# Performance work log

Hardware: AMD Instinct MI355X
Metric: run time of the kernel (lower is better)

Reference implementation:

```python
import jax, jax.numpy as jnp
import numpy as np

B, S, D, H = 4, 2048, 768, 12
HD = D // H
SCALE = HD ** -0.5


def setup_inputs() -> dict:
    key = jax.random.key(0)
    ks = jax.random.split(key, 9)
    std = D ** -0.5
    x = jax.random.normal(ks[0], (B, S, D), dtype=jnp.float32)
    Wq = jax.random.normal(ks[1], (D, D), dtype=jnp.float32) * std
    Wk = jax.random.normal(ks[2], (D, D), dtype=jnp.float32) * std
    Wv = jax.random.normal(ks[3], (D, D), dtype=jnp.float32) * std
    Wo = jax.random.normal(ks[4], (D, D), dtype=jnp.float32) * std
    bq = jax.random.normal(ks[5], (D,), dtype=jnp.float32) * 0.01
    bk = jax.random.normal(ks[6], (D,), dtype=jnp.float32) * 0.01
    bv = jax.random.normal(ks[7], (D,), dtype=jnp.float32) * 0.01
    bo = jax.random.normal(ks[8], (D,), dtype=jnp.float32) * 0.01
    return {"x": x, "Wq": Wq, "bq": bq, "Wk": Wk, "bk": bk,
            "Wv": Wv, "bv": bv, "Wo": Wo, "bo": bo}


def reference(x, Wq, bq, Wk, bk, Wv, bv, Wo, bo):
    b, s, _ = x.shape
    # projections (torch Linear: y = x @ W.T + b)
    q = (x @ Wq.T + bq).reshape(b, s, H, HD).transpose(0, 2, 1, 3)  # [B,H,S,HD]
    k = (x @ Wk.T + bk).reshape(b, s, H, HD).transpose(0, 2, 1, 3)
    v = (x @ Wv.T + bv).reshape(b, s, H, HD).transpose(0, 2, 1, 3)
    attn = jnp.einsum('bhqd,bhkd->bhqk', q, k) * SCALE
    attn = jax.nn.softmax(attn, axis=-1)  # dropout is identity in eval mode
    out = jnp.einsum('bhqk,bhkd->bhqd', attn, v)
    out = out.transpose(0, 2, 1, 3).reshape(b, s, D)
    return out @ Wo.T + bo
```

## Files before the change

### kernel.cpp

```cpp
#include <hip/hip_runtime.h>

#define LOG2E 1.4426950408889634f
#define QSCALE (0.125f * LOG2E)

typedef __attribute__((ext_vector_type(8))) __bf16 bf8_t;
typedef __attribute__((ext_vector_type(4))) float f4_t;

__device__ __forceinline__ unsigned short f2bf(float f) {
  unsigned int u = __float_as_uint(f);
  u += 0x7fff + ((u >> 16) & 1);
  return (unsigned short)(u >> 16);
}

__device__ __forceinline__ void async16(const void* g, void* l) {
  __builtin_amdgcn_global_load_lds(
      (const __attribute__((address_space(1))) void*)g,
      (__attribute__((address_space(3))) void*)l, 16, 0, 0);
}

__device__ __forceinline__ int swm(int r) {
  return ((r & 3) << 4) | ((r & 8) << 3);
}
__device__ __forceinline__ int swzoff(int row, int cb) {
  return (row << 7) + (cb ^ swm(row));
}

__global__ void cvt_multi(const float* __restrict__ x,
                          const float* __restrict__ w0, const float* __restrict__ w1,
                          const float* __restrict__ w2, const float* __restrict__ w3,
                          unsigned short* __restrict__ xb,
                          unsigned short* __restrict__ d0, unsigned short* __restrict__ d1,
                          unsigned short* __restrict__ d2, unsigned short* __restrict__ d3) {
  const int NX = 1572864;
  const int NW = 147456;
  const int total = NX + 4 * NW;
  int i = blockIdx.x * blockDim.x + threadIdx.x;
  int stride = gridDim.x * blockDim.x;
  for (; i < total; i += stride) {
    const float* s;
    unsigned short* d;
    int off;
    if (i < NX) {
      s = x; d = xb; off = i;
    } else {
      int j = i - NX;
      int wsel = j / NW;
      off = j - wsel * NW;
      s = (wsel == 0) ? w0 : (wsel == 1) ? w1 : (wsel == 2) ? w2 : w3;
      d = (wsel == 0) ? d0 : (wsel == 1) ? d1 : (wsel == 2) ? d2 : d3;
    }
    float4 v = ((const float4*)s)[off];
    ushort4 o;
    o.x = f2bf(v.x); o.y = f2bf(v.y); o.z = f2bf(v.z); o.w = f2bf(v.w);
    ((ushort4*)d)[off] = o;
  }
}

__device__ __forceinline__ void gemm_core(const unsigned short* __restrict__ A,
                                          const unsigned short* __restrict__ Bm,
                                          int i0, int j0, char* ls,
                                          f4_t (&acc)[4][4]) {
  const int tid = threadIdx.x;
  const int l = tid & 63;
  const int wi = (tid >> 6) >> 1, wj = (tid >> 6) & 1;
  auto stage = [&](int buf, int k0) {
    char* dA = ls + buf * 32768;
    char* dB = dA + 16384;
#pragma unroll
    for (int u = 0; u < 4; ++u) {
      int p = (u * 256 + tid) * 16;
      int r = p >> 7, c = (p & 127) ^ swm(r);
      async16((const char*)A + ((size_t)(i0 + r) * 768 + k0) * 2 + c, dA + p);
      async16((const char*)Bm + ((size_t)(j0 + r) * 768 + k0) * 2 + c, dB + p);
    }
  };
  stage(0, 0);
  __syncthreads();
  for (int kk = 0; kk < 12; ++kk) {
    if (kk < 11) stage((kk + 1) & 1, (kk + 1) * 64);
    const char* lsA = ls + (kk & 1) * 32768;
    const char* lsB = lsA + 16384;
#pragma unroll
    for (int ks = 0; ks < 2; ++ks) {
      bf8_t af[4], bfr[4];
#pragma unroll
      for (int mi = 0; mi < 4; ++mi)
        af[mi] = *(const bf8_t*)(lsA + swzoff(wi * 64 + mi * 16 + (l & 15),
                                              ks * 64 + ((l >> 4) << 4)));
#pragma unroll
      for (int nj = 0; nj < 4; ++nj)
        bfr[nj] = *(const bf8_t*)(lsB + swzoff(wj * 64 + nj * 16 + (l & 15),
                                               ks * 64 + ((l >> 4) << 4)));
      __builtin_amdgcn_s_setprio(1);
#pragma unroll
      for (int mi = 0; mi < 4; ++mi)
#pragma unroll
        for (int nj = 0; nj < 4; ++nj)
          acc[mi][nj] = __builtin_amdgcn_mfma_f32_16x16x32_bf16(
              af[mi], bfr[nj], acc[mi][nj], 0, 0, 0);
      __builtin_amdgcn_s_setprio(0);
    }
    __syncthreads();
  }
}

__global__ __launch_bounds__(256) void proj_qkv(
    const unsigned short* __restrict__ xb,
    const unsigned short* __restrict__ wq,
    const unsigned short* __restrict__ wk,
    const unsigned short* __restrict__ wv,
    const float* __restrict__ bq, const float* __restrict__ bk,
    const float* __restrict__ bv,
    unsigned short* __restrict__ qo, unsigned short* __restrict__ ko,
    unsigned short* __restrict__ vto) {
  __shared__ char ls[65536];
  const int bx = (blockIdx.x & 7) * 144 + (blockIdx.x >> 3);
  const int mt = bx / 18, nt = bx % 18;
  const int sec = nt / 6, nn = nt % 6;
  const int nbase = nn * 128;
  const int mbase = mt * 128;
  const unsigned short *A, *Bm;
  if (sec == 0)      { A = wq; Bm = xb; }
  else if (sec == 1) { A = wk; Bm = xb; }
  else               { A = xb; Bm = wv; }
  const int gi0 = (sec == 2) ? mbase : nbase;
  const int gj0 = (sec == 2) ? nbase : mbase;
  f4_t acc[4][4] = {};
  gemm_core(A, Bm, gi0, gj0, ls, acc);

  const int tid = threadIdx.x, l = tid & 63;
  const int wi = (tid >> 6) >> 1, wj = (tid >> 6) & 1;
#pragma unroll
  for (int mi = 0; mi < 4; ++mi) {
#pragma unroll
    for (int nj = 0; nj < 4; ++nj) {
      int ib = wi * 64 + mi * 16 + ((l >> 4) << 2);
      int j  = wj * 64 + nj * 16 + (l & 15);
      f4_t v = acc[mi][nj];
      ushort4 o;
      if (sec < 2) {
        const float* bias = sec ? bk : bq;
        float sc = sec ? 1.0f : QSCALE;
        float4 bs = *(const float4*)(bias + nbase + ib);
        o.x = f2bf((v[0] + bs.x) * sc);
        o.y = f2bf((v[1] + bs.y) * sc);
        o.z = f2bf((v[2] + bs.z) * sc);
        o.w = f2bf((v[3] + bs.w) * sc);
      } else {
        float bvs = bv[nbase + j];
        o.x = f2bf(v[0] + bvs); o.y = f2bf(v[1] + bvs);
        o.z = f2bf(v[2] + bvs); o.w = f2bf(v[3] + bvs);
      }
      int chunk = (ib >> 3) ^ (j & 15);
      *(ushort4*)(ls + j * 256 + chunk * 16 + ((ib & 7) << 1)) = o;
    }
  }
  __syncthreads();
  const int row = tid >> 1, half = tid & 1;
  if (sec < 2) {
    int sg = mbase + row;
    int b = sg >> 11, s = sg & 2047;
    int h = nn * 2 + half;
    unsigned short* dst = (sec ? ko : qo) + (((size_t)(b * 12 + h) * 2048 + s) << 6);
#pragma unroll
    for (int c = 0; c < 8; ++c) {
      int cb = half * 8 + c;
      uint4 v = *(const uint4*)(ls + row * 256 + ((cb ^ (row & 15)) << 4));
      ((uint4*)dst)[c] = v;
    }
  } else {
    int h = nn * 2 + (row >> 6), dh = row & 63;
    int b = mt >> 4;
    int scol = (mt & 15) * 128 + half * 64;
    unsigned short* dst = vto + ((size_t)((b * 12 + h) * 64 + dh)) * 2048 + scol;
#pragma unroll
    for (int c = 0; c < 8; ++c) {
      int cb = half * 8 + c;
      uint4 v = *(const uint4*)(ls + row * 256 + ((cb ^ (row & 15)) << 4));
      ((uint4*)dst)[c] = v;
    }
  }
}

__global__ __launch_bounds__(256) void proj_o(
    const unsigned short* __restrict__ attnb, const unsigned short* __restrict__ wo,
    const float* __restrict__ bo, float* __restrict__ outp) {
  __shared__ char ls[65536];
  const int bx = (blockIdx.x & 7) * 48 + (blockIdx.x >> 3);
  const int it = bx % 6, jt = bx / 6;
  const int i0 = it * 128, j0 = jt * 128;
  f4_t acc[4][4] = {};
  gemm_core(wo, attnb, i0, j0, ls, acc);
  const int tid = threadIdx.x, l = tid & 63;
  const int wi = (tid >> 6) >> 1, wj = (tid >> 6) & 1;
#pragma unroll
  for (int mi = 0; mi < 4; ++mi) {
#pragma unroll
    for (int nj = 0; nj < 4; ++nj) {
      int ib = i0 + wi * 64 + mi * 16 + ((l >> 4) << 2);
      int j  = j0 + wj * 64 + nj * 16 + (l & 15);
      float4 bs = *(const float4*)(bo + ib);
      float4 o;
      o.x = acc[mi][nj][0] + bs.x;
      o.y = acc[mi][nj][1] + bs.y;
      o.z = acc[mi][nj][2] + bs.z;
      o.w = acc[mi][nj][3] + bs.w;
      *(float4*)(outp + (size_t)j * 768 + ib) = o;
    }
  }
}

__global__ __launch_bounds__(512) void attn_kernel(
    const unsigned short* __restrict__ qg,
    const unsigned short* __restrict__ kg,
    const unsigned short* __restrict__ vtg,
    unsigned short* __restrict__ attnb) {
  __shared__ char ls[65536];
  const int tid = threadIdx.x, l = tid & 63, w = tid >> 6;
  const int qw = w & 3, hf = w >> 2;
  const int swz = (blockIdx.x & 7) * 96 + (blockIdx.x >> 3);
  const int q0 = (swz & 15) * 128;
  const int bh = swz >> 4;
  const size_t qkbase = (size_t)bh * 2048 * 64;
  const size_t vtbase = (size_t)bh * 64 * 2048;

#pragma unroll
  for (int u = 0; u < 2; ++u) {
    int p = (u * 512 + tid) * 16;
    int r = p >> 7, cb = p & 127;
    int c = cb ^ swm(r);
    async16((const char*)qg + (qkbase + (size_t)(q0 + r) * 64) * 2 + c, ls + p);
  }
  __syncthreads();
  bf8_t qf[2][2];
#pragma unroll
  for (int qt = 0; qt < 2; ++qt)
#pragma unroll
    for (int ks = 0; ks < 2; ++ks)
      qf[qt][ks] = *(const bf8_t*)(ls + swzoff(qw * 32 + qt * 16 + (l & 15),
                                               ks * 64 + ((l >> 4) << 4)));
  __syncthreads();

  const int p16 = tid * 16;
  const int sr = p16 >> 7;
  const int sc = (p16 & 127) ^ swm(sr);
  async16((const char*)kg + (qkbase + (size_t)sr * 64) * 2 + sc, ls + p16);
  async16((const char*)vtg + (vtbase + (size_t)sr * 2048) * 2 + sc,
          ls + 8192 + p16);
  async16((const char*)kg + (qkbase + (size_t)(64 + sr) * 64) * 2 + sc,
          ls + 16384 + p16);
  async16((const char*)vtg + (vtbase + (size_t)sr * 2048 + 64) * 2 + sc,
          ls + 16384 + 8192 + p16);
  const char* gKa = (const char*)kg + (qkbase + (size_t)(128 + sr) * 64) * 2 + sc;
  const char* gVa = (const char*)vtg + (vtbase + (size_t)sr * 2048 + 128) * 2 + sc;
  const char* gKb = gKa + 8192;
  const char* gVb = gVa + 128;
  __syncthreads();

  int koff[4][2];
#pragma unroll
  for (int kt = 0; kt < 4; ++kt) {
    int i = l & 15;
    int row = ((kt >> 1) << 5) + ((kt & 1) << 2) + ((i >> 2) << 3) + (i & 3);
#pragma unroll
    for (int ks = 0; ks < 2; ++ks)
      koff[kt][ks] = swzoff(row, ks * 64 + ((l >> 4) << 4));
  }
  int voff[4][2];
#pragma unroll
  for (int dt = 0; dt < 4; ++dt)
#pragma unroll
    for (int ks = 0; ks < 2; ++ks)
      voff[dt][ks] = swzoff(dt * 16 + (l & 15), ks * 64 + ((l >> 4) << 4));

  bf8_t onesf;
#pragma unroll
  for (int e = 0; e < 8; ++e) onesf[e] = (__bf16)1.0f;

  f4_t acc[4][2] = {};
  f4_t accs[2] = {};

  for (int i = 0; i < 16; ++i) {
    if (i < 15) {
      char* dst = ls + (((i + 1) & 1) * 2) * 16384;
      async16(gKa, dst + p16);
      async16(gVa, dst + 8192 + p16);
      async16(gKb, dst + 16384 + p16);
      async16(gVb, dst + 16384 + 8192 + p16);
      gKa += 16384; gKb += 16384;
      gVa += 256;   gVb += 256;
    }
    const char* bK = ls + ((i & 1) * 2 + hf) * 16384;
    const char* bV = bK + 8192;

    f4_t sacc[4][2] = {};
    __builtin_amdgcn_s_setprio(1);
#pragma unroll
    for (int kt = 0; kt < 4; ++kt)
#pragma unroll
      for (int ks = 0; ks < 2; ++ks) {
        bf8_t a = *(const bf8_t*)(bK + koff[kt][ks]);
#pragma unroll
        for (int qt = 0; qt < 2; ++qt)
          sacc[kt][qt] = __builtin_amdgcn_mfma_f32_16x16x32_bf16(
              a, qf[qt][ks], sacc[kt][qt], 0, 0, 0);
      }
    __builtin_amdgcn_s_setprio(0);

    bf8_t pf[2][2];
#pragma unroll
    for (int qt = 0; qt < 2; ++qt)
#pragma unroll
      for (int ks = 0; ks < 2; ++ks)
#pragma unroll
        for (int e = 0; e < 8; ++e)
          pf[ks][qt][e] =
              (__bf16)__builtin_amdgcn_exp2f(sacc[2 * ks + (e >> 2)][qt][e & 3]);

    __builtin_amdgcn_s_setprio(1);
#pragma unroll
    for (int dt = 0; dt < 4; ++dt) {
      bf8_t av0 = *(const bf8_t*)(bV + voff[dt][0]);
      bf8_t av1 = *(const bf8_t*)(bV + voff[dt][1]);
#pragma unroll
      for (int qt = 0; qt < 2; ++qt) {
        acc[dt][qt] = __builtin_amdgcn_mfma_f32_16x16x32_bf16(av0, pf[0][qt],
                                                              acc[dt][qt], 0, 0, 0);
        acc[dt][qt] = __builtin_amdgcn_mfma_f32_16x16x32_bf16(av1, pf[1][qt],
                                                              acc[dt][qt], 0, 0, 0);
      }
    }
#pragma unroll
    for (int qt = 0; qt < 2; ++qt) {
      accs[qt] = __builtin_amdgcn_mfma_f32_16x16x32_bf16(onesf, pf[0][qt],
                                                         accs[qt], 0, 0, 0);
      accs[qt] = __builtin_amdgcn_mfma_f32_16x16x32_bf16(onesf, pf[1][qt],
                                                         accs[qt], 0, 0, 0);
    }
    __builtin_amdgcn_s_setprio(0);
    __syncthreads();
  }

  char* reg_ = ls + qw * 8704;
  if (hf) {
#pragma unroll
    for (int dt = 0; dt < 4; ++dt)
#pragma unroll
      for (int qt = 0; qt < 2; ++qt)
        *(f4_t*)(reg_ + (((dt * 2 + qt) * 64) + l) * 16) = acc[dt][qt];
    *(float2*)(reg_ + 8192 + l * 8) = float2{accs[0][0], accs[1][0]};
  }
  __syncthreads();
  if (!hf) {
    const int bb = bh / 12, h = bh % 12;
    float2 os = *(const float2*)(reg_ + 8192 + l * 8);
    float inv0 = 1.0f / (accs[0][0] + os.x);
    float inv1 = 1.0f / (accs[1][0] + os.y);
#pragma unroll
    for (int qt = 0; qt < 2; ++qt) {
      float inv = qt ? inv1 : inv0;
      int s = q0 + qw * 32 + qt * 16 + (l & 15);
#pragma unroll
      for (int dt = 0; dt < 4; ++dt) {
        f4_t other = *(const f4_t*)(reg_ + (((dt * 2 + qt) * 64) + l) * 16);
        int dg = h * 64 + dt * 16 + ((l >> 4) << 2);
        ushort4 o;
        o.x = f2bf((acc[dt][qt][0] + other[0]) * inv);
        o.y = f2bf((acc[dt][qt][1] + other[1]) * inv);
        o.z = f2bf((acc[dt][qt][2] + other[2]) * inv);
        o.w = f2bf((acc[dt][qt][3] + other[3]) * inv);
        *(ushort4*)(attnb + ((size_t)(bb * 2048 + s)) * 768 + dg) = o;
      }
    }
  }
}

extern "C" void kernel_launch(void* const* d_in, const int* in_sizes, int n_in,
                              void* d_out, int out_size, void* d_ws, size_t ws_size,
                              hipStream_t stream) {
  const float* x  = (const float*)d_in[0];
  const float* Wq = (const float*)d_in[1];
  const float* bq = (const float*)d_in[2];
  const float* Wk = (const float*)d_in[3];
  const float* bk = (const float*)d_in[4];
  const float* Wv = (const float*)d_in[5];
  const float* bv = (const float*)d_in[6];
  const float* Wo = (const float*)d_in[7];
  const float* bo = (const float*)d_in[8];

  const size_t XB_ELEMS = (size_t)8192 * 768;
  const size_t W_ELEMS  = (size_t)768 * 768;
  unsigned short* xb  = (unsigned short*)d_ws;
  unsigned short* wqb = xb  + XB_ELEMS;
  unsigned short* wkb = wqb + W_ELEMS;
  unsigned short* wvb = wkb + W_ELEMS;
  unsigned short* wob = wvb + W_ELEMS;
  unsigned short* qb  = wob + W_ELEMS;
  unsigned short* kb  = qb  + XB_ELEMS;
  unsigned short* vtb = kb  + XB_ELEMS;
  unsigned short* attnb = xb;

  cvt_multi<<<2048, 256, 0, stream>>>(x, Wq, Wk, Wv, Wo,
                                      xb, wqb, wkb, wvb, wob);
  proj_qkv<<<1152, 256, 0, stream>>>(xb, wqb, wkb, wvb, bq, bk, bv, qb, kb, vtb);
  attn_kernel<<<768, 512, 0, stream>>>(qb, kb, vtb, attnb);
  proj_o<<<384, 256, 0, stream>>>(attnb, wob, bo, (float*)d_out);
}
```

Before: 138.1 us.

## Fuse fp32-to-bf16 conversion of x into QKV projection GEMM loads

The x activation is no longer converted to bf16 in a separate kernel. The QKV projection now loads fp32 x tiles into registers, converts them to bf16 and writes them into swizzled LDS, overlapping this with the MFMA work, while weights still use async LDS loads. This removes the full bf16 write and re-read of x, but each x tile is now read in fp32 by all 18 column tiles, which raises global read traffic. The shared gemm_core also replaces __syncthreads with explicit vmcnt waits plus s_barrier.

```diff
diff --git a/kernel.cpp b/kernel.cpp
--- a/kernel.cpp
+++ b/kernel.cpp
@@ -25,34 +25,102 @@
   return (row << 7) + (cb ^ swm(row));
 }
 
-__global__ void cvt_multi(const float* __restrict__ x,
-                          const float* __restrict__ w0, const float* __restrict__ w1,
-                          const float* __restrict__ w2, const float* __restrict__ w3,
-                          unsigned short* __restrict__ xb,
-                          unsigned short* __restrict__ d0, unsigned short* __restrict__ d1,
-                          unsigned short* __restrict__ d2, unsigned short* __restrict__ d3) {
-  const int NX = 1572864;
-  const int NW = 147456;
-  const int total = NX + 4 * NW;
+__global__ void cvt4_kernel(const float* __restrict__ s0, const float* __restrict__ s1,
+                            const float* __restrict__ s2, const float* __restrict__ s3,
+                            unsigned short* __restrict__ d0, unsigned short* __restrict__ d1,
+                            unsigned short* __restrict__ d2, unsigned short* __restrict__ d3,
+                            int n4) {
+  int z = blockIdx.y;
+  const float* s = (z == 0) ? s0 : (z == 1) ? s1 : (z == 2) ? s2 : s3;
+  unsigned short* d = (z == 0) ? d0 : (z == 1) ? d1 : (z == 2) ? d2 : d3;
   int i = blockIdx.x * blockDim.x + threadIdx.x;
   int stride = gridDim.x * blockDim.x;
-  for (; i < total; i += stride) {
-    const float* s;
-    unsigned short* d;
-    int off;
-    if (i < NX) {
-      s = x; d = xb; off = i;
-    } else {
-      int j = i - NX;
-      int wsel = j / NW;
-      off = j - wsel * NW;
-      s = (wsel == 0) ? w0 : (wsel == 1) ? w1 : (wsel == 2) ? w2 : w3;
-      d = (wsel == 0) ? d0 : (wsel == 1) ? d1 : (wsel == 2) ? d2 : d3;
-    }
-    float4 v = ((const float4*)s)[off];
+  for (; i < n4; i += stride) {
+    float4 v = ((const float4*)s)[i];
     ushort4 o;
     o.x = f2bf(v.x); o.y = f2bf(v.y); o.z = f2bf(v.z); o.w = f2bf(v.w);
-    ((ushort4*)d)[off] = o;
+    ((ushort4*)d)[i] = o;
+  }
+}
+
+template <bool XA>
+__device__ __forceinline__ void gemm_core_x(const unsigned short* __restrict__ W,
+                                            const float* __restrict__ X,
+                                            int i0, int j0, char* ls,
+                                            f4_t (&acc)[4][4]) {
+  const int tid = threadIdx.x, l = tid & 63;
+  const int wi = (tid >> 6) >> 1, wj = (tid >> 6) & 1;
+  const int xrb = XA ? i0 : j0;
+  const int wrb = XA ? j0 : i0;
+  const int xhalf = XA ? 0 : 16384;
+  float4 xr[4][2];
+  auto xload = [&](int k0) {
+#pragma unroll
+    for (int u = 0; u < 4; ++u) {
+      int o2 = (u * 256 + tid) * 16;
+      int r = o2 >> 7, cbb = o2 & 127;
+      const float* g = X + (size_t)(xrb + r) * 768 + k0 + (cbb >> 1);
+      xr[u][0] = *(const float4*)g;
+      xr[u][1] = *(const float4*)(g + 4);
+    }
+  };
+  auto xwrite = [&](int buf) {
+    char* dX = ls + buf * 32768 + xhalf;
+#pragma unroll
+    for (int u = 0; u < 4; ++u) {
+      int o2 = (u * 256 + tid) * 16;
+      int r = o2 >> 7, cbb = o2 & 127;
+      uint4 v;
+      v.x = f2bf(xr[u][0].x) | ((unsigned)f2bf(xr[u][0].y) << 16);
+      v.y = f2bf(xr[u][0].z) | ((unsigned)f2bf(xr[u][0].w) << 16);
+      v.z = f2bf(xr[u][1].x) | ((unsigned)f2bf(xr[u][1].y) << 16);
+      v.w = f2bf(xr[u][1].z) | ((unsigned)f2bf(xr[u][1].w) << 16);
+      *(uint4*)(dX + (r << 7) + (cbb ^ swm(r))) = v;
+    }
+  };
+  auto wstage = [&](int buf, int k0) {
+    char* dW = ls + buf * 32768 + (16384 - xhalf);
+#pragma unroll
+    for (int u = 0; u < 4; ++u) {
+      int p = (u * 256 + tid) * 16;
+      int r = p >> 7, c = (p & 127) ^ swm(r);
+      async16((const char*)W + ((size_t)(wrb + r) * 768 + k0) * 2 + c, dW + p);
+    }
+  };
+  xload(0);
+  wstage(0, 0);
+  xwrite(0);
+  __syncthreads();
+  for (int kk = 0; kk < 12; ++kk) {
+    const int buf = kk & 1;
+    if (kk < 11) {
+      wstage(buf ^ 1, (kk + 1) * 64);
+      xload((kk + 1) * 64);
+    }
+    const char* lsA = ls + buf * 32768;
+    const char* lsB = lsA + 16384;
+#pragma unroll
+    for (int ks = 0; ks < 2; ++ks) {
+      bf8_t af[4], bfr[4];
+#pragma unroll
+      for (int mi = 0; mi < 4; ++mi)
+        af[mi] = *(const bf8_t*)(lsA + swzoff(wi * 64 + mi * 16 + (l & 15),
+                                              ks * 64 + ((l >> 4) << 4)));
+#pragma unroll
+      for (int nj = 0; nj < 4; ++nj)
+        bfr[nj] = *(const bf8_t*)(lsB + swzoff(wj * 64 + nj * 16 + (l & 15),
+                                               ks * 64 + ((l >> 4) << 4)));
+      __builtin_amdgcn_s_setprio(1);
+#pragma unroll
+      for (int mi = 0; mi < 4; ++mi)
+#pragma unroll
+        for (int nj = 0; nj < 4; ++nj)
+          acc[mi][nj] = __builtin_amdgcn_mfma_f32_16x16x32_bf16(
+              af[mi], bfr[nj], acc[mi][nj], 0, 0, 0);
+      __builtin_amdgcn_s_setprio(0);
+    }
+    if (kk < 11) xwrite(buf ^ 1);
+    __syncthreads();
   }
 }
 
@@ -75,9 +143,14 @@
     }
   };
   stage(0, 0);
-  __syncthreads();
   for (int kk = 0; kk < 12; ++kk) {
-    if (kk < 11) stage((kk + 1) & 1, (kk + 1) * 64);
+    if (kk < 11) {
+      stage((kk + 1) & 1, (kk + 1) * 64);
+      asm volatile("s_waitcnt vmcnt(8)" ::: "memory");
+    } else {
+      asm volatile("s_waitcnt vmcnt(0)" ::: "memory");
+    }
+    __builtin_amdgcn_s_barrier();
     const char* lsA = ls + (kk & 1) * 32768;
     const char* lsB = lsA + 16384;
 #pragma unroll
@@ -100,12 +173,12 @@
               af[mi], bfr[nj], acc[mi][nj], 0, 0, 0);
       __builtin_amdgcn_s_setprio(0);
     }
-    __syncthreads();
+    __builtin_amdgcn_s_barrier();
   }
 }
 
 __global__ __launch_bounds__(256) void proj_qkv(
-    const unsigned short* __restrict__ xb,
+    const float* __restrict__ xf,
     const unsigned short* __restrict__ wq,
     const unsigned short* __restrict__ wk,
     const unsigned short* __restrict__ wv,
@@ -119,14 +192,10 @@
   const int sec = nt / 6, nn = nt % 6;
   const int nbase = nn * 128;
   const int mbase = mt * 128;
-  const unsigned short *A, *Bm;
-  if (sec == 0)      { A = wq; Bm = xb; }
-  else if (sec == 1) { A = wk; Bm = xb; }
-  else               { A = xb; Bm = wv; }
-  const int gi0 = (sec == 2) ? mbase : nbase;
-  const int gj0 = (sec == 2) ? nbase : mbase;
   f4_t acc[4][4] = {};
-  gemm_core(A, Bm, gi0, gj0, ls, acc);
+  if (sec == 0)      gemm_core_x<false>(wq, xf, nbase, mbase, ls, acc);
+  else if (sec == 1) gemm_core_x<false>(wk, xf, nbase, mbase, ls, acc);
+  else               gemm_core_x<true>(wv, xf, mbase, nbase, ls, acc);
 
   const int tid = threadIdx.x, l = tid & 63;
   const int wi = (tid >> 6) >> 1, wj = (tid >> 6) & 1;
@@ -390,19 +459,19 @@
 
   const size_t XB_ELEMS = (size_t)8192 * 768;
   const size_t W_ELEMS  = (size_t)768 * 768;
-  unsigned short* xb  = (unsigned short*)d_ws;
-  unsigned short* wqb = xb  + XB_ELEMS;
+  unsigned short* wqb = (unsigned short*)d_ws;
   unsigned short* wkb = wqb + W_ELEMS;
   unsigned short* wvb = wkb + W_ELEMS;
   unsigned short* wob = wvb + W_ELEMS;
   unsigned short* qb  = wob + W_ELEMS;
   unsigned short* kb  = qb  + XB_ELEMS;
   unsigned short* vtb = kb  + XB_ELEMS;
-  unsigned short* attnb = xb;
-
-  cvt_multi<<<2048, 256, 0, stream>>>(x, Wq, Wk, Wv, Wo,
-                                      xb, wqb, wkb, wvb, wob);
-  proj_qkv<<<1152, 256, 0, stream>>>(xb, wqb, wkb, wvb, bq, bk, bv, qb, kb, vtb);
+  unsigned short* attnb = vtb + XB_ELEMS;
+
+  cvt4_kernel<<<dim3(144, 4), 256, 0, stream>>>(Wq, Wk, Wv, Wo,
+                                                wqb, wkb, wvb, wob,
+                                                (int)(W_ELEMS / 4));
+  proj_qkv<<<1152, 256, 0, stream>>>(x, wqb, wkb, wvb, bq, bk, bv, qb, kb, vtb);
   attn_kernel<<<768, 512, 0, stream>>>(qb, kb, vtb, attnb);
   proj_o<<<384, 256, 0, stream>>>(attnb, wob, bo, (float*)d_out);
 }
```

Result: slower. 149.2 us (+8.0%).
